# Kernel tuning notes

Hardware: AMD Instinct MI355X
Metric: run time of the kernel (lower is better)

The kernel has to match this reference:

```python
import jax, jax.numpy as jnp
import numpy as np

N_INP = 256
N_OUT = 16
H = 1024
UH = 32  # uni_hidden_unit
BATCH = 16384


def setup_inputs() -> dict:
    key = jax.random.key(0)
    ks = jax.random.split(key, 16)
    s = 0.02
    return {
        "x": jax.random.normal(ks[0], (BATCH, N_INP), dtype=jnp.float32),
        # main MLP: n_inp -> 1024 -> 1024 -> n_out
        "W0": jax.random.normal(ks[1], (N_INP, H), dtype=jnp.float32) * s,
        "b0": jnp.zeros((H,), jnp.float32),
        "W1": jax.random.normal(ks[2], (H, H), dtype=jnp.float32) * s,
        "b1": jnp.zeros((H,), jnp.float32),
        "W2": jax.random.normal(ks[3], (H, N_OUT), dtype=jnp.float32) * s,
        "b2": jnp.zeros((N_OUT,), jnp.float32),
        # stacked per-feature uni MLPs: 1 -> UH -> UH -> n_out, one per feature
        "uw1": jax.random.normal(ks[4], (N_INP, UH), dtype=jnp.float32) * s,
        "ub1": jnp.zeros((N_INP, UH), jnp.float32),
        "uw2": jax.random.normal(ks[5], (N_INP, UH, UH), dtype=jnp.float32) * s,
        "ub2": jnp.zeros((N_INP, UH), jnp.float32),
        "uw3": jax.random.normal(ks[6], (N_INP, UH, N_OUT), dtype=jnp.float32) * s,
        "ub3": jnp.zeros((N_INP, N_OUT), jnp.float32),
    }


def reference(x, W0, b0, W1, b1, W2, b2, uw1, ub1, uw2, ub2, uw3, ub3):
    # main MLP: Linear+ReLU, Linear+ReLU, Linear
    y = jax.nn.relu(x @ W0 + b0)
    y = jax.nn.relu(y @ W1 + b1)
    y = y @ W2 + b2  # [B, n_out]

    # per-feature univariate MLPs, vectorized over the feature axis i
    # input to uni MLP i is x[:, i:i+1]  -> first Linear(1, UH)
    h = jax.nn.relu(x[:, :, None] * uw1[None] + ub1[None])       # [B, I, UH]
    h = jax.nn.relu(jnp.einsum('bif,ifo->bio', h, uw2) + ub2[None])  # [B, I, UH]
    u = jnp.einsum('bif,ifo->bio', h, uw3) + ub3[None]           # [B, I, n_out]
    return y + u.sum(axis=1)
```

## Files before the change

kernel.cpp:

```cpp
#include <hip/hip_runtime.h>

typedef unsigned short u16;
typedef __attribute__((ext_vector_type(4))) float f32x4;
typedef __attribute__((ext_vector_type(4))) int i32x4;
typedef __attribute__((ext_vector_type(8))) __bf16 bf16x8;
typedef __attribute__((ext_vector_type(4))) unsigned short u16x4;

#define BATCH 16384
#define NINP 256
#define HID 1024
#define NOUT 16

__device__ __forceinline__ u16 f2bf(float f) {
  unsigned u = __builtin_bit_cast(unsigned, f);
  u += 0x7FFFu + ((u >> 16) & 1u);
  return (u16)(u >> 16);
}
__device__ __forceinline__ f32x4 mfma_bb(bf16x8 a, bf16x8 b, f32x4 c) {
  return __builtin_amdgcn_mfma_f32_16x16x32_bf16(a, b, c, 0, 0, 0);
}
__device__ __forceinline__ void gload_lds16(const void* g, void* l) {
  __builtin_amdgcn_global_load_lds(
      (const __attribute__((address_space(1))) void*)g,
      (__attribute__((address_space(3))) void*)l, 16, 0, 0);
}

static const size_t OFF_H0   = 0;
static const size_t OFF_PART = 0;
static const size_t OFF_H1   = 33554432;
static const size_t OFF_XB   = 33554432;
static const size_t OFF_W0T  = 67108864;
static const size_t OFF_W1T  = 67633152;
static const size_t OFF_W2T  = 69730304;
static const size_t OFF_UWP  = 69763072;
static const size_t OFF_CB   = 70811648;

__global__ __launch_bounds__(256) void k_prep(
    const float* __restrict__ x,
    const float* __restrict__ W0, const float* __restrict__ W1,
    const float* __restrict__ W2,
    const float* __restrict__ uw1, const float* __restrict__ ub1,
    const float* __restrict__ uw2, const float* __restrict__ ub2,
    const float* __restrict__ uw3, const float* __restrict__ b2,
    const float* __restrict__ ub3,
    u16* __restrict__ xb,
    u16* __restrict__ W0T, u16* __restrict__ W1T, u16* __restrict__ W2T,
    char* __restrict__ uwp, float* __restrict__ cb)
{
  __shared__ float tile[32][33];
  const int bid = blockIdx.x;
  const int tid = threadIdx.x;

  if (bid < 1312) {
    const float* src; u16* dst; int K, N, kb, ob;
    if (bid < 256)       { src = W0; dst = W0T; K = 256;  N = 1024; int t = bid;        kb = (t & 7) * 32;  ob = (t >> 3) * 32; }
    else if (bid < 1280) { src = W1; dst = W1T; K = 1024; N = 1024; int t = bid - 256;  kb = (t & 31) * 32; ob = (t >> 5) * 32; }
    else                 { src = W2; dst = W2T; K = 1024; N = 16;   int t = bid - 1280; kb = t * 32;        ob = 0; }
    const int tx = tid & 31, ty = tid >> 5;
    for (int r = ty; r < 32; r += 8)
      if (ob + tx < N) tile[r][tx] = src[(size_t)(kb + r) * N + ob + tx];
    __syncthreads();
    for (int r = ty; r < 32; r += 8)
      if (ob + r < N) dst[(size_t)(ob + r) * K + kb + tx] = f2bf(tile[tx][r]);
  } else if (bid < 5408) {
    const int idx = ((bid - 1312) * 256 + tid) * 4;
    const float4 v = *(const float4*)&x[idx];
    u16x4 o4 = { f2bf(v.x), f2bf(v.y), f2bf(v.z), f2bf(v.w) };
    *(u16x4*)&xb[idx] = o4;
  } else if (bid < 5664) {
    const int e = ((bid - 5408) * 256 + tid) * 4;
    const float4 v = *(const float4*)&uw2[e];
    const int i = e >> 10, f = (e >> 5) & 31, o = e & 31;
    const float vv[4] = { v.x, v.y, v.z, v.w };
    u16* blob16 = (u16*)(uwp + (size_t)i * 4096);
#pragma unroll
    for (int d = 0; d < 4; ++d) {
      const int oo = o + d;
      const int lane = ((f >> 3) << 4) | (oo & 15);
      blob16[256 + (oo >> 4) * 512 + lane * 8 + (f & 7)] = f2bf(vv[d]);
    }
  } else if (bid < 5792) {
    const int e = ((bid - 5664) * 256 + tid) * 4;
    const float4 v = *(const float4*)&uw3[e];
    const int i = e >> 9, f = (e >> 4) & 31, o2 = e & 15;
    const int s = (f < 16) ? (((f >> 2) << 3) + (f & 3))
                           : ((((f - 16) >> 2) << 3) + 4 + (f & 3));
    const float vv[4] = { v.x, v.y, v.z, v.w };
    u16* blob16 = (u16*)(uwp + (size_t)i * 4096);
#pragma unroll
    for (int d = 0; d < 4; ++d)
      blob16[1280 + ((s >> 3) * 16 + o2 + d) * 8 + (s & 7)] = f2bf(vv[d]);
  } else if (bid < 5816) {
    const int e4 = (bid - 5792) * 256 + tid;
    const int i = e4 / 24, r4 = e4 % 24;
    const float* src = (r4 < 8)  ? &uw1[i * 32 + r4 * 4]
                     : (r4 < 16) ? &ub1[i * 32 + (r4 - 8) * 4]
                                 : &ub2[i * 32 + (r4 - 16) * 4];
    *(float4*)(uwp + (size_t)i * 4096 + r4 * 16) = *(const float4*)src;
  } else {
    __shared__ float red[16][16];
    const int ig = tid >> 4, o = tid & 15;
    float s = 0.f;
#pragma unroll
    for (int k = 0; k < 16; ++k) s += ub3[(ig * 16 + k) * 16 + o];
    red[ig][o] = s;
    __syncthreads();
    if (tid < 16) {
      float t = b2[tid];
#pragma unroll
      for (int k = 0; k < 16; ++k) t += red[k][tid];
      cb[tid] = t;
    }
  }
}

__global__ __launch_bounds__(512, 2) void k_gemm8(
    const u16* __restrict__ A, const u16* __restrict__ BT,
    const float* __restrict__ bias, u16* __restrict__ C,
    int M, int N, int K)
{
  extern __shared__ __align__(16) char lds[];
  const int tid = threadIdx.x;
  const int lane = tid & 63, wid = tid >> 6;
  const int l15 = lane & 15, g = lane >> 4;
  const int wA = wid >> 2;
  const int wn = wid & 3;
  const int nbn = N >> 8;
  int logical = blockIdx.x;
  { const int nwg = gridDim.x;
    if ((nwg & 7) == 0) { const int q = nwg >> 3; logical = (logical & 7) * q + (logical >> 3); } }
  const int bm = logical / nbn, bn = logical - bm * nbn;
  const size_t rb = (size_t)bm * 256, cb = (size_t)bn * 256;

  const int q7 = l15 & 7;
  const int arow0 = wA * 128 + l15;
  const int brow0 = wn * 64 + l15;

  char* const ldsA = lds;
  char* const ldsB = lds + 65536;

  const u16* Ag = A + rb * K;
  const u16* Bg = BT + cb * K;

  float bv[4];
#pragma unroll
  for (int n = 0; n < 4; ++n) bv[n] = bias[cb + wn * 64 + n * 16 + l15];

  f32x4 acc[8][4] = {};
  const int NT = K >> 6;

#define STAGE(arr, src, ktE, s) do { \
    const int G_ = (s) * 512 + tid; \
    const int row_ = G_ >> 3; \
    const int c8_ = (G_ & 7) ^ (row_ & 7); \
    gload_lds16(&(src)[(size_t)row_ * K + (ktE) + c8_ * 8], (arr) + G_ * 16); \
  } while (0)

#define ARD(bp, m, kk) (*(const bf16x8*)((bp) + (((arow0 + (m) * 16) * 8 + (((kk) * 4 + g) ^ q7)) << 4)))
#define BRD(bp, n, kk) (*(const bf16x8*)((bp) + (((brow0 + (n) * 16) * 8 + (((kk) * 4 + g) ^ q7)) << 4)))

  STAGE(ldsB, Bg, 0, 0); STAGE(ldsB, Bg, 0, 1);
  STAGE(ldsB, Bg, 0, 2); STAGE(ldsB, Bg, 0, 3);
  STAGE(ldsA, Ag, 0, 0); STAGE(ldsA, Ag, 0, 2);
  STAGE(ldsA, Ag, 0, 1); STAGE(ldsA, Ag, 0, 3);
  asm volatile("s_waitcnt vmcnt(2)" ::: "memory");
  __builtin_amdgcn_s_barrier();

  for (int t = 0; t < NT; ++t) {
    const int b = t & 1;
    const char* Ab = ldsA + b * 32768;
    const char* Bb = ldsB + b * 32768;
    char* An = ldsA + (b ^ 1) * 32768;
    char* Bn = ldsB + (b ^ 1) * 32768;
    const int tn = (t + 1 < NT) ? t + 1 : 0;
    const int kt1 = tn << 6;
    bf16x8 av[4][2], bv0[2][2], bv1[2][2];

#pragma unroll
    for (int m = 0; m < 4; ++m) { av[m][0] = ARD(Ab, m, 0); av[m][1] = ARD(Ab, m, 1); }
#pragma unroll
    for (int n = 0; n < 2; ++n) { bv0[n][0] = BRD(Bb, n, 0); bv0[n][1] = BRD(Bb, n, 1); }
    STAGE(Bn, Bg, kt1, 0); STAGE(Bn, Bg, kt1, 1);
    __builtin_amdgcn_s_barrier();
    __builtin_amdgcn_s_setprio(1);
#pragma unroll
    for (int m = 0; m < 4; ++m)
#pragma unroll
      for (int n = 0; n < 2; ++n) {
        acc[m][n] = mfma_bb(av[m][0], bv0[n][0], acc[m][n]);
        acc[m][n] = mfma_bb(av[m][1], bv0[n][1], acc[m][n]);
      }
    __builtin_amdgcn_s_setprio(0);
    __builtin_amdgcn_s_barrier();

#pragma unroll
    for (int n = 0; n < 2; ++n) { bv1[n][0] = BRD(Bb, n + 2, 0); bv1[n][1] = BRD(Bb, n + 2, 1); }
    STAGE(Bn, Bg, kt1, 2); STAGE(Bn, Bg, kt1, 3);
    __builtin_amdgcn_s_barrier();
    __builtin_amdgcn_s_setprio(1);
#pragma unroll
    for (int m = 0; m < 4; ++m)
#pragma unroll
      for (int n = 0; n < 2; ++n) {
        acc[m][n + 2] = mfma_bb(av[m][0], bv1[n][0], acc[m][n + 2]);
        acc[m][n + 2] = mfma_bb(av[m][1], bv1[n][1], acc[m][n + 2]);
      }
    __builtin_amdgcn_s_setprio(0);
    asm volatile("s_waitcnt vmcnt(4)" ::: "memory");
    __builtin_amdgcn_s_barrier();

#pragma unroll
    for (int m = 0; m < 4; ++m) { av[m][0] = ARD(Ab, m + 4, 0); av[m][1] = ARD(Ab, m + 4, 1); }
    STAGE(An, Ag, kt1, 0); STAGE(An, Ag, kt1, 2);
    __builtin_amdgcn_s_barrier();
    __builtin_amdgcn_s_setprio(1);
#pragma unroll
    for (int m = 0; m < 4; ++m)
#pragma unroll
      for (int n = 0; n < 2; ++n) {
        acc[m + 4][n + 2] = mfma_bb(av[m][0], bv1[n][0], acc[m + 4][n + 2]);
        acc[m + 4][n + 2] = mfma_bb(av[m][1], bv1[n][1], acc[m + 4][n + 2]);
      }
    __builtin_amdgcn_s_setprio(0);
    __builtin_amdgcn_s_barrier();

    STAGE(An, Ag, kt1, 1); STAGE(An, Ag, kt1, 3);
    __builtin_amdgcn_s_setprio(1);
#pragma unroll
    for (int m = 0; m < 4; ++m)
#pragma unroll
      for (int n = 0; n < 2; ++n) {
        acc[m + 4][n] = mfma_bb(av[m][0], bv0[n][0], acc[m + 4][n]);
        acc[m + 4][n] = mfma_bb(av[m][1], bv0[n][1], acc[m + 4][n]);
      }
    __builtin_amdgcn_s_setprio(0);
    asm volatile("s_waitcnt vmcnt(2)" ::: "memory");
    __builtin_amdgcn_s_barrier();
  }
#undef STAGE
#undef ARD
#undef BRD

  asm volatile("s_waitcnt vmcnt(0)" ::: "memory");

  {
    char* const ep = lds;
#pragma unroll
    for (int h = 0; h < 2; ++h) {
      __syncthreads();
#pragma unroll
      for (int mloc = 0; mloc < 4; ++mloc)
#pragma unroll
        for (int n = 0; n < 4; ++n) {
          const int col = wn * 64 + n * 16 + l15;
#pragma unroll
          for (int r = 0; r < 4; ++r) {
            const int lrow = wA * 64 + mloc * 16 + g * 4 + r;
            *(u16*)(ep + lrow * 512 + ((col * 2) ^ ((lrow & 7) << 4))) =
                f2bf(fmaxf(acc[h * 4 + mloc][n][r] + bv[n], 0.f));
          }
        }
      __syncthreads();
#pragma unroll
      for (int p = 0; p < 8; ++p) {
        const int ci = p * 512 + tid;
        const int lrow = ci >> 5, c16 = ci & 31;
        const i32x4 v = *(const i32x4*)(ep + lrow * 512 + ((c16 * 16) ^ ((lrow & 7) << 4)));
        const int grow = (int)rb + (lrow >> 6) * 128 + h * 64 + (lrow & 63);
        *(i32x4*)&C[(size_t)grow * N + cb + c16 * 8] = v;
      }
    }
  }
}

__global__ __launch_bounds__(256, 4) void k_uni(
    const float* __restrict__ x,
    const char* __restrict__ uwp,
    const u16* __restrict__ H1, const u16* __restrict__ W2T,
    float* __restrict__ part)
{
  const int tid = threadIdx.x, lane = tid & 63, wid = tid >> 6;
  const int l15 = lane & 15, g = lane >> 4;
  const int chunk = blockIdx.x & 7, rowblk = blockIdx.x >> 3;
  const int rb_blk = rowblk * 128;
  const int rb = rb_blk + wid * 32;
  const int i0 = chunk * 32;

  __shared__ __align__(16) float xt[128][33];
  __shared__ __align__(16) char wbuf[2][4096];

  {
    const int r0 = tid >> 3, c4 = (tid & 7) << 2;
#pragma unroll
    for (int rr = 0; rr < 128; rr += 32)
      *(float4*)&xt[rr + r0][c4] =
          *(const float4*)&x[(size_t)(rb_blk + rr + r0) * NINP + i0 + c4];
  }
  gload_lds16(uwp + (size_t)i0 * 4096 + tid * 16, &wbuf[0][tid * 16]);
  __syncthreads();

  const f32x4 zero4 = {0.f, 0.f, 0.f, 0.f};
  f32x4 acc0 = zero4, acc1 = zero4;
  const float* xr0 = &xt[wid * 32 + l15][0];
  const float* xr1 = &xt[wid * 32 + 16 + l15][0];

#pragma unroll 2
  for (int ii = 0; ii < 32; ++ii) {
    const int nxt = (ii + 1) & 31;
    gload_lds16(uwp + (size_t)(i0 + nxt) * 4096 + tid * 16,
                &wbuf[(ii + 1) & 1][tid * 16]);

    const char* bp = &wbuf[ii & 1][0];
    const f32x4 w1lo = *(const f32x4*)(bp + g * 32);
    const f32x4 w1hi = *(const f32x4*)(bp + g * 32 + 16);
    const f32x4 b1lo = *(const f32x4*)(bp + 128 + g * 32);
    const f32x4 b1hi = *(const f32x4*)(bp + 128 + g * 32 + 16);
    const f32x4 bb0  = *(const f32x4*)(bp + 256 + g * 16);
    const f32x4 bb1  = *(const f32x4*)(bp + 320 + g * 16);
    const bf16x8 bv0 = *(const bf16x8*)(bp + 512 + lane * 16);
    const bf16x8 bv1 = *(const bf16x8*)(bp + 1536 + lane * 16);
    const bf16x8 b3  = *(const bf16x8*)(bp + 2560 + lane * 16);
    const float xv0 = xr0[ii], xv1 = xr1[ii];

    bf16x8 af0, af1;
#pragma unroll
    for (int j = 0; j < 4; ++j) {
      af0[j]     = (__bf16)fmaxf(fmaf(xv0, w1lo[j], b1lo[j]), 0.f);
      af0[4 + j] = (__bf16)fmaxf(fmaf(xv0, w1hi[j], b1hi[j]), 0.f);
      af1[j]     = (__bf16)fmaxf(fmaf(xv1, w1lo[j], b1lo[j]), 0.f);
      af1[4 + j] = (__bf16)fmaxf(fmaf(xv1, w1hi[j], b1hi[j]), 0.f);
    }

    const f32x4 d00 = mfma_bb(bv0, af0, bb0);
    const f32x4 d10 = mfma_bb(bv1, af0, bb1);
    const f32x4 d01 = mfma_bb(bv0, af1, bb0);
    const f32x4 d11 = mfma_bb(bv1, af1, bb1);

    bf16x8 h20, h21;
#pragma unroll
    for (int j = 0; j < 4; ++j) {
      h20[j]     = (__bf16)fmaxf(d00[j], 0.f);
      h20[4 + j] = (__bf16)fmaxf(d10[j], 0.f);
      h21[j]     = (__bf16)fmaxf(d01[j], 0.f);
      h21[4 + j] = (__bf16)fmaxf(d11[j], 0.f);
    }

    acc0 = mfma_bb(b3, h20, acc0);
    acc1 = mfma_bb(b3, h21, acc1);

    __syncthreads();
  }

  {
    const int kb0 = chunk * 128;
#pragma unroll
    for (int kk = 0; kk < 4; ++kk) {
      const int kb = kb0 + kk * 32;
      const bf16x8 a0 = __builtin_bit_cast(bf16x8,
          *(const i32x4*)&H1[(size_t)(rb + l15) * HID + kb + g * 8]);
      const bf16x8 a1 = __builtin_bit_cast(bf16x8,
          *(const i32x4*)&H1[(size_t)(rb + 16 + l15) * HID + kb + g * 8]);
      const bf16x8 bv = __builtin_bit_cast(bf16x8,
          *(const i32x4*)&W2T[l15 * HID + kb + g * 8]);
      acc0 = mfma_bb(bv, a0, acc0);
      acc1 = mfma_bb(bv, a1, acc1);
    }
  }

  float* p = part + ((size_t)chunk * BATCH + rb) * NOUT;
  *(f32x4*)&p[l15 * 16 + g * 4] = acc0;
  *(f32x4*)&p[(16 + l15) * 16 + g * 4] = acc1;
}

__global__ __launch_bounds__(256) void k_reduce(
    const float* __restrict__ part, const float* __restrict__ cb,
    float* __restrict__ out)
{
  const int j4 = blockIdx.x * 256 + threadIdx.x;
  const float4 c = ((const float4*)cb)[j4 & 3];
  const float4* p = (const float4*)part;
  float rx = c.x, ry = c.y, rz = c.z, rw = c.w;
#pragma unroll
  for (int cc = 0; cc < 8; ++cc) {
    const float4 a = p[cc * 65536 + j4];
    rx += a.x; ry += a.y; rz += a.z; rw += a.w;
  }
  float4 r; r.x = rx; r.y = ry; r.z = rz; r.w = rw;
  ((float4*)out)[j4] = r;
}

extern "C" void kernel_launch(void* const* d_in, const int* in_sizes, int n_in,
                              void* d_out, int out_size, void* d_ws, size_t ws_size,
                              hipStream_t stream) {
  (void)in_sizes; (void)n_in; (void)out_size; (void)ws_size;
  const float* x   = (const float*)d_in[0];
  const float* W0  = (const float*)d_in[1];
  const float* b0  = (const float*)d_in[2];
  const float* W1  = (const float*)d_in[3];
  const float* b1  = (const float*)d_in[4];
  const float* W2  = (const float*)d_in[5];
  const float* b2  = (const float*)d_in[6];
  const float* uw1 = (const float*)d_in[7];
  const float* ub1 = (const float*)d_in[8];
  const float* uw2 = (const float*)d_in[9];
  const float* ub2 = (const float*)d_in[10];
  const float* uw3 = (const float*)d_in[11];
  const float* ub3 = (const float*)d_in[12];
  float* out = (float*)d_out;

  char* ws = (char*)d_ws;
  u16*   H0   = (u16*)(ws + OFF_H0);
  u16*   H1   = (u16*)(ws + OFF_H1);
  u16*   xb   = (u16*)(ws + OFF_XB);
  u16*   W0T  = (u16*)(ws + OFF_W0T);
  u16*   W1T  = (u16*)(ws + OFF_W1T);
  u16*   W2T  = (u16*)(ws + OFF_W2T);
  char*  uwp  = (char*)(ws + OFF_UWP);
  float* cb   = (float*)(ws + OFF_CB);
  float* part = (float*)(ws + OFF_PART);

  hipFuncSetAttribute((const void*)k_gemm8,
                      hipFuncAttributeMaxDynamicSharedMemorySize, 131072);

  k_prep<<<5817, 256, 0, stream>>>(x, W0, W1, W2, uw1, ub1, uw2, ub2, uw3,
                                   b2, ub3, xb, W0T, W1T, W2T, uwp, cb);
  k_gemm8<<<256, 512, 131072, stream>>>(xb, W0T, b0, H0, BATCH, HID, NINP);
  k_gemm8<<<256, 512, 131072, stream>>>(H0, W1T, b1, H1, BATCH, HID, HID);
  k_uni<<<1024, 256, 0, stream>>>(x, uwp, H1, W2T, part);
  k_reduce<<<256, 256, 0, stream>>>(part, cb, out);
}
```

Measured before the change: 99.36 us.

## Fuse final W2 projection into second GEMM epilogue, drop H1 round-trip

The second hidden-layer GEMM no longer writes the 16384x1024 bf16 H1 activation to memory. Its epilogue multiplies each 256-column tile by the matching slice of W2 with MFMA and writes per-column-block fp32 partial sums. The uni kernel stops reading H1, and the reduce kernel adds the four extra partials. The K dimension also becomes a template constant. This removes a large activation write and read, at the cost of extra partial-buffer traffic and register pressure from the preloaded W2 fragments in the GEMM.

```diff
diff --git a/kernel.cpp b/kernel.cpp
--- a/kernel.cpp
+++ b/kernel.cpp
@@ -25,15 +25,15 @@
       (__attribute__((address_space(3))) void*)l, 16, 0, 0);
 }
 
-static const size_t OFF_H0   = 0;
-static const size_t OFF_PART = 0;
-static const size_t OFF_H1   = 33554432;
-static const size_t OFF_XB   = 33554432;
-static const size_t OFF_W0T  = 67108864;
-static const size_t OFF_W1T  = 67633152;
-static const size_t OFF_W2T  = 69730304;
-static const size_t OFF_UWP  = 69763072;
-static const size_t OFF_CB   = 70811648;
+static const size_t OFF_H0    = 0;
+static const size_t OFF_PARTU = 0;
+static const size_t OFF_XB    = 33554432;
+static const size_t OFF_PARTF = 33554432;
+static const size_t OFF_W0T   = 67108864;
+static const size_t OFF_W1T   = 67633152;
+static const size_t OFF_W2T   = 69730304;
+static const size_t OFF_UWP   = 69763072;
+static const size_t OFF_CB    = 70811648;
 
 __global__ __launch_bounds__(256) void k_prep(
     const float* __restrict__ x,
@@ -114,10 +114,11 @@
   }
 }
 
+template<int KT, bool FOLD>
 __global__ __launch_bounds__(512, 2) void k_gemm8(
     const u16* __restrict__ A, const u16* __restrict__ BT,
     const float* __restrict__ bias, u16* __restrict__ C,
-    int M, int N, int K)
+    const u16* __restrict__ W2Tp, float* __restrict__ pfold, int N)
 {
   extern __shared__ __align__(16) char lds[];
   const int tid = threadIdx.x;
@@ -139,21 +140,28 @@
   char* const ldsA = lds;
   char* const ldsB = lds + 65536;
 
-  const u16* Ag = A + rb * K;
-  const u16* Bg = BT + cb * K;
-
+  const u16* Ag = A + rb * KT;
+  const u16* Bg = BT + cb * KT;
+
+  bf16x8 w2f[8];
+  if constexpr (FOLD) {
+#pragma unroll
+    for (int c = 0; c < 8; ++c)
+      w2f[c] = __builtin_bit_cast(bf16x8,
+          *(const i32x4*)&W2Tp[l15 * HID + (int)cb + c * 32 + g * 8]);
+  }
   float bv[4];
 #pragma unroll
   for (int n = 0; n < 4; ++n) bv[n] = bias[cb + wn * 64 + n * 16 + l15];
 
   f32x4 acc[8][4] = {};
-  const int NT = K >> 6;
+  const int NT = KT >> 6;
 
 #define STAGE(arr, src, ktE, s) do { \
     const int G_ = (s) * 512 + tid; \
     const int row_ = G_ >> 3; \
     const int c8_ = (G_ & 7) ^ (row_ & 7); \
-    gload_lds16(&(src)[(size_t)row_ * K + (ktE) + c8_ * 8], (arr) + G_ * 16); \
+    gload_lds16(&(src)[(size_t)row_ * KT + (ktE) + c8_ * 8], (arr) + G_ * 16); \
   } while (0)
 
 #define ARD(bp, m, kk) (*(const bf16x8*)((bp) + (((arow0 + (m) * 16) * 8 + (((kk) * 4 + g) ^ q7)) << 4)))
@@ -261,13 +269,29 @@
           }
         }
       __syncthreads();
-#pragma unroll
-      for (int p = 0; p < 8; ++p) {
-        const int ci = p * 512 + tid;
-        const int lrow = ci >> 5, c16 = ci & 31;
-        const i32x4 v = *(const i32x4*)(ep + lrow * 512 + ((c16 * 16) ^ ((lrow & 7) << 4)));
-        const int grow = (int)rb + (lrow >> 6) * 128 + h * 64 + (lrow & 63);
-        *(i32x4*)&C[(size_t)grow * N + cb + c16 * 8] = v;
+      if constexpr (!FOLD) {
+#pragma unroll
+        for (int p = 0; p < 8; ++p) {
+          const int ci = p * 512 + tid;
+          const int lrow = ci >> 5, c16 = ci & 31;
+          const i32x4 v = *(const i32x4*)(ep + lrow * 512 + ((c16 * 16) ^ ((lrow & 7) << 4)));
+          const int grow = (int)rb + (lrow >> 6) * 128 + h * 64 + (lrow & 63);
+          *(i32x4*)&C[(size_t)grow * N + cb + c16 * 8] = v;
+        }
+      } else {
+        const int lrow = wid * 16 + l15;
+        f32x4 accf = {0.f, 0.f, 0.f, 0.f};
+#pragma unroll
+        for (int c = 0; c < 8; ++c) {
+          const bf16x8 afr = *(const bf16x8*)(
+              ep + lrow * 512 + ((c * 64 + g * 16) ^ ((lrow & 7) << 4)));
+          accf = mfma_bb(afr, w2f[c], accf);
+        }
+        const int rowb2 = (int)rb + (wid >> 2) * 128 + h * 64 + (wid & 3) * 16;
+        float* pf = pfold + ((size_t)bn * BATCH + rowb2) * NOUT;
+#pragma unroll
+        for (int r = 0; r < 4; ++r)
+          pf[(g * 4 + r) * NOUT + l15] = accf[r];
       }
     }
   }
@@ -276,7 +300,6 @@
 __global__ __launch_bounds__(256, 4) void k_uni(
     const float* __restrict__ x,
     const char* __restrict__ uwp,
-    const u16* __restrict__ H1, const u16* __restrict__ W2T,
     float* __restrict__ part)
 {
   const int tid = threadIdx.x, lane = tid & 63, wid = tid >> 6;
@@ -351,38 +374,28 @@
     __syncthreads();
   }
 
-  {
-    const int kb0 = chunk * 128;
-#pragma unroll
-    for (int kk = 0; kk < 4; ++kk) {
-      const int kb = kb0 + kk * 32;
-      const bf16x8 a0 = __builtin_bit_cast(bf16x8,
-          *(const i32x4*)&H1[(size_t)(rb + l15) * HID + kb + g * 8]);
-      const bf16x8 a1 = __builtin_bit_cast(bf16x8,
-          *(const i32x4*)&H1[(size_t)(rb + 16 + l15) * HID + kb + g * 8]);
-      const bf16x8 bv = __builtin_bit_cast(bf16x8,
-          *(const i32x4*)&W2T[l15 * HID + kb + g * 8]);
-      acc0 = mfma_bb(bv, a0, acc0);
-      acc1 = mfma_bb(bv, a1, acc1);
-    }
-  }
-
   float* p = part + ((size_t)chunk * BATCH + rb) * NOUT;
   *(f32x4*)&p[l15 * 16 + g * 4] = acc0;
   *(f32x4*)&p[(16 + l15) * 16 + g * 4] = acc1;
 }
 
 __global__ __launch_bounds__(256) void k_reduce(
-    const float* __restrict__ part, const float* __restrict__ cb,
-    float* __restrict__ out)
+    const float* __restrict__ pu, const float* __restrict__ pf,
+    const float* __restrict__ cb, float* __restrict__ out)
 {
   const int j4 = blockIdx.x * 256 + threadIdx.x;
   const float4 c = ((const float4*)cb)[j4 & 3];
-  const float4* p = (const float4*)part;
+  const float4* a4 = (const float4*)pu;
+  const float4* b4 = (const float4*)pf;
   float rx = c.x, ry = c.y, rz = c.z, rw = c.w;
 #pragma unroll
   for (int cc = 0; cc < 8; ++cc) {
-    const float4 a = p[cc * 65536 + j4];
+    const float4 a = a4[cc * 65536 + j4];
+    rx += a.x; ry += a.y; rz += a.z; rw += a.w;
+  }
+#pragma unroll
+  for (int cc = 0; cc < 4; ++cc) {
+    const float4 a = b4[cc * 65536 + j4];
     rx += a.x; ry += a.y; rz += a.z; rw += a.w;
   }
   float4 r; r.x = rx; r.y = ry; r.z = rz; r.w = rw;
@@ -409,23 +422,27 @@
   float* out = (float*)d_out;
 
   char* ws = (char*)d_ws;
-  u16*   H0   = (u16*)(ws + OFF_H0);
-  u16*   H1   = (u16*)(ws + OFF_H1);
-  u16*   xb   = (u16*)(ws + OFF_XB);
-  u16*   W0T  = (u16*)(ws + OFF_W0T);
-  u16*   W1T  = (u16*)(ws + OFF_W1T);
-  u16*   W2T  = (u16*)(ws + OFF_W2T);
-  char*  uwp  = (char*)(ws + OFF_UWP);
-  float* cb   = (float*)(ws + OFF_CB);
-  float* part = (float*)(ws + OFF_PART);
-
-  hipFuncSetAttribute((const void*)k_gemm8,
+  u16*   H0    = (u16*)(ws + OFF_H0);
+  u16*   xb    = (u16*)(ws + OFF_XB);
+  u16*   W0T   = (u16*)(ws + OFF_W0T);
+  u16*   W1T   = (u16*)(ws + OFF_W1T);
+  u16*   W2T   = (u16*)(ws + OFF_W2T);
+  char*  uwp   = (char*)(ws + OFF_UWP);
+  float* cb    = (float*)(ws + OFF_CB);
+  float* partu = (float*)(ws + OFF_PARTU);
+  float* partf = (float*)(ws + OFF_PARTF);
+
+  hipFuncSetAttribute((const void*)k_gemm8<256, false>,
+                      hipFuncAttributeMaxDynamicSharedMemorySize, 131072);
+  hipFuncSetAttribute((const void*)k_gemm8<1024, true>,
                       hipFuncAttributeMaxDynamicSharedMemorySize, 131072);
 
   k_prep<<<5817, 256, 0, stream>>>(x, W0, W1, W2, uw1, ub1, uw2, ub2, uw3,
                                    b2, ub3, xb, W0T, W1T, W2T, uwp, cb);
-  k_gemm8<<<256, 512, 131072, stream>>>(xb, W0T, b0, H0, BATCH, HID, NINP);
-  k_gemm8<<<256, 512, 131072, stream>>>(H0, W1T, b1, H1, BATCH, HID, HID);
-  k_uni<<<1024, 256, 0, stream>>>(x, uwp, H1, W2T, part);
-  k_reduce<<<256, 256, 0, stream>>>(part, cb, out);
-}
+  k_gemm8<256, false><<<256, 512, 131072, stream>>>(
+      xb, W0T, b0, H0, nullptr, nullptr, HID);
+  k_gemm8<1024, true><<<256, 512, 131072, stream>>>(
+      H0, W1T, b1, nullptr, W2T, partf, HID);
+  k_uni<<<1024, 256, 0, stream>>>(x, uwp, partu);
+  k_reduce<<<256, 256, 0, stream>>>(partu, partf, cb, out);
+}
```

Result: no change. 100.6 us (+1.3%).
